# Performance work log

Hardware: AMD Instinct MI355X
Metric: run time of the kernel (lower is better)

## Reference

```python
import jax, jax.numpy as jnp
import numpy as np

B, S, H = 16, 4096, 1024

def setup_inputs() -> dict:
    key = jax.random.key(0)
    k1, k2, k3, k4 = jax.random.split(key, 4)
    hidden_states = jax.random.normal(k1, (B, S, H), dtype=jnp.float32)
    query_indices = jnp.sort(jax.random.randint(k2, (B, 2), 0, S), axis=1).astype(jnp.int64)
    attention_mask = jax.random.uniform(k3, (B,), dtype=jnp.float32)
    w = jax.random.normal(k4, (H,), dtype=jnp.float32) / jnp.sqrt(jnp.float32(H))
    return {"hidden_states": hidden_states, "query_indices": query_indices,
            "attention_mask": attention_mask, "w": w}

def reference(hidden_states, query_indices, attention_mask, w):
    # attention_mask is [B]; original broadcasts it over seq and hidden dims.
    hs = hidden_states * attention_mask[:, None, None]                  # [B,S,H]
    start = query_indices[:, 0]                                         # [B]
    end = query_indices[:, 1]                                           # [B]
    qlen = end - start                                                  # arange(start,end) length
    max_len = jnp.max(end + 1 - start)                                  # original pads to max(end-start+1)
    j = jnp.arange(S)                                                   # static padded query axis
    valid = j[None, :] < qlen[:, None]                                  # real gathered positions
    included = j[None, :] < max_len                                     # positions inside padded window
    idx = jnp.where(valid, start[:, None] + j[None, :], 0)              # [B,S]
    gathered = jnp.take_along_axis(hs, idx[:, :, None], axis=1)         # [B,S,H]
    gathered = gathered * valid[:, :, None].astype(hs.dtype)            # zero padded rows
    scores = jnp.einsum('bsh,h->bs', gathered, w)                       # padded-included rows score 0
    scores = jnp.where(included, scores, -jnp.inf)                      # beyond max_len: excluded
    attn = jax.nn.softmax(scores, axis=1)                               # [B,S]
    return jnp.einsum('bs,bsh->bh', attn, gathered)                     # [B,H]
```

## Files before the change

### kernel.cpp

```cpp
#include <hip/hip_runtime.h>
#include <math.h>

#define BB 16
#define SS 4096
#define HH 1024

__global__ __launch_bounds__(256) void score_kernel(
    const float* __restrict__ hidden,
    const int*   __restrict__ qidx,
    const float* __restrict__ mask,
    const float* __restrict__ w,
    float*       __restrict__ scores)
{
    const int b     = blockIdx.y;
    const int start = qidx[2 * b];
    const int qlen  = qidx[2 * b + 1] - start;
    const int lane  = threadIdx.x & 63;
    const int wave  = threadIdx.x >> 6;
    const int j     = blockIdx.x * 4 + wave;
    if (blockIdx.x * 4 >= qlen) return;
    if (j >= qlen) return;

    const float4* row =
        (const float4*)(hidden + ((size_t)b * SS + start + j) * HH);
    const float4* wv = (const float4*)w;

    float acc = 0.f;
#pragma unroll
    for (int k = 0; k < 4; ++k) {
        float4 hv = row[lane + 64 * k];
        float4 wr = wv[lane + 64 * k];
        acc += hv.x * wr.x + hv.y * wr.y + hv.z * wr.z + hv.w * wr.w;
    }
#pragma unroll
    for (int off = 32; off > 0; off >>= 1)
        acc += __shfl_down(acc, off, 64);
    if (lane == 0) scores[b * SS + j] = acc * mask[b];
}

__global__ __launch_bounds__(256) void softmax_kernel(
    const int*   __restrict__ qidx,
    const float* __restrict__ mask,
    float*       __restrict__ scores,
    float*       __restrict__ out)
{
    const int b     = blockIdx.x;
    const int start = qidx[2 * b];
    const int qlen  = qidx[2 * b + 1] - start;

    int max_len = 0;
    for (int i = 0; i < BB; ++i) {
        int l = qidx[2 * i + 1] - qidx[2 * i];
        max_len = max(max_len, l);
    }
    max_len += 1;

    const int tid  = threadIdx.x;
    const int lane = tid & 63;
    const int wave = tid >> 6;

    ((float4*)out)[b * (HH / 4) + tid] = make_float4(0.f, 0.f, 0.f, 0.f);

    __shared__ float red[8];

    float m = -INFINITY;
    for (int j = tid; j < qlen; j += 256) m = fmaxf(m, scores[b * SS + j]);
#pragma unroll
    for (int off = 32; off > 0; off >>= 1)
        m = fmaxf(m, __shfl_down(m, off, 64));
    if (lane == 0) red[wave] = m;
    __syncthreads();
    if (tid == 0) {
        float mm = fmaxf(fmaxf(red[0], red[1]), fmaxf(red[2], red[3]));
        red[0] = fmaxf(mm, 0.f);
    }
    __syncthreads();
    m = red[0];
    __syncthreads();

    float s = 0.f;
    for (int j = tid; j < qlen; j += 256) s += __expf(scores[b * SS + j] - m);
#pragma unroll
    for (int off = 32; off > 0; off >>= 1) s += __shfl_down(s, off, 64);
    if (lane == 0) red[wave] = s;
    __syncthreads();
    if (tid == 0) {
        float denom = red[0] + red[1] + red[2] + red[3];
        denom += (float)(max_len - qlen) * __expf(-m);
        red[4] = mask[b] / denom;
    }
    __syncthreads();
    const float scale = red[4];

    for (int j = tid; j < qlen; j += 256)
        scores[b * SS + j] = __expf(scores[b * SS + j] - m) * scale;
}

__global__ __launch_bounds__(256) void agg_kernel(
    const float* __restrict__ hidden,
    const int*   __restrict__ qidx,
    const float* __restrict__ weights,
    float*       __restrict__ out)
{
    const int b     = blockIdx.y;
    const int start = qidx[2 * b];
    const int qlen  = qidx[2 * b + 1] - start;
    const int j0    = blockIdx.x * 16;
    if (j0 >= qlen) return;
    const int jend = min(j0 + 16, qlen);
    const int tid  = threadIdx.x;

    const float4* base =
        (const float4*)(hidden + ((size_t)b * SS + start) * HH) + tid;

    float4 acc = make_float4(0.f, 0.f, 0.f, 0.f);
#pragma unroll 4
    for (int j = j0; j < jend; ++j) {
        const float wt = weights[b * SS + j];
        float4 hv = base[(size_t)j * (HH / 4)];
        acc.x += wt * hv.x;
        acc.y += wt * hv.y;
        acc.z += wt * hv.z;
        acc.w += wt * hv.w;
    }
    float* o = out + b * HH + tid * 4;
    atomicAdd(o + 0, acc.x);
    atomicAdd(o + 1, acc.y);
    atomicAdd(o + 2, acc.z);
    atomicAdd(o + 3, acc.w);
}

extern "C" void kernel_launch(void* const* d_in, const int* in_sizes, int n_in,
                              void* d_out, int out_size, void* d_ws, size_t ws_size,
                              hipStream_t stream)
{
    const float* hidden = (const float*)d_in[0];
    const int*   qidx   = (const int*)d_in[1];
    const float* mask   = (const float*)d_in[2];
    const float* w      = (const float*)d_in[3];
    float*       out    = (float*)d_out;
    float*       scores = (float*)d_ws;

    score_kernel<<<dim3(SS / 4, BB), 256, 0, stream>>>(hidden, qidx, mask, w, scores);
    softmax_kernel<<<BB, 256, 0, stream>>>(qidx, mask, scores, out);
    agg_kernel<<<dim3(SS / 16, BB), 256, 0, stream>>>(hidden, qidx, scores, out);
}
```

Measured before the change: 345.9 us.

## Fuse scoring, softmax and aggregation into single-pass partial sums

Replaces the three-kernel score/softmax/aggregate pipeline with one pass. Each wave computes a row's score, exponentiates it and accumulates the weighted row and the denominator while the row is still in registers. A small second kernel then reduces the per-block partials. Hidden states are read once instead of twice and the atomics are removed. In exchange, the max subtraction in softmax is dropped, so very large scores could overflow, and the partials need extra workspace.

```diff
diff --git a/kernel.cpp b/kernel.cpp
--- a/kernel.cpp
+++ b/kernel.cpp
@@ -4,49 +4,90 @@
 #define BB 16
 #define SS 4096
 #define HH 1024
+#define CH 64
+#define NWB (CH * 4)
 
-__global__ __launch_bounds__(256) void score_kernel(
+__global__ __launch_bounds__(256) void pass1_kernel(
     const float* __restrict__ hidden,
     const int*   __restrict__ qidx,
     const float* __restrict__ mask,
     const float* __restrict__ w,
-    float*       __restrict__ scores)
+    float4*      __restrict__ pnum,
+    float*       __restrict__ pden)
 {
     const int b     = blockIdx.y;
     const int start = qidx[2 * b];
     const int qlen  = qidx[2 * b + 1] - start;
     const int lane  = threadIdx.x & 63;
     const int wave  = threadIdx.x >> 6;
-    const int j     = blockIdx.x * 4 + wave;
-    if (blockIdx.x * 4 >= qlen) return;
-    if (j >= qlen) return;
+    const int wid   = blockIdx.x * 4 + wave;
+    const float mb  = mask[b];
 
-    const float4* row =
-        (const float4*)(hidden + ((size_t)b * SS + start + j) * HH);
-    const float4* wv = (const float4*)w;
+    float4 wreg[4];
+#pragma unroll
+    for (int k = 0; k < 4; ++k)
+        wreg[k] = ((const float4*)w)[lane + 64 * k];
 
-    float acc = 0.f;
+    float4 acc[4];
 #pragma unroll
-    for (int k = 0; k < 4; ++k) {
-        float4 hv = row[lane + 64 * k];
-        float4 wr = wv[lane + 64 * k];
-        acc += hv.x * wr.x + hv.y * wr.y + hv.z * wr.z + hv.w * wr.w;
+    for (int k = 0; k < 4; ++k) acc[k] = make_float4(0.f, 0.f, 0.f, 0.f);
+    float dacc = 0.f;
+
+    for (int j = wid; j < qlen; j += NWB) {
+        const float4* row =
+            (const float4*)(hidden + ((size_t)b * SS + start + j) * HH);
+        float4 hv[4];
+        float s = 0.f;
+#pragma unroll
+        for (int k = 0; k < 4; ++k) {
+            hv[k] = row[lane + 64 * k];
+            s += hv[k].x * wreg[k].x + hv[k].y * wreg[k].y +
+                 hv[k].z * wreg[k].z + hv[k].w * wreg[k].w;
+        }
+#pragma unroll
+        for (int off = 32; off > 0; off >>= 1)
+            s += __shfl_down(s, off, 64);
+        s = __shfl(s, 0, 64);
+        const float e = __expf(s * mb);
+        dacc += e;
+#pragma unroll
+        for (int k = 0; k < 4; ++k) {
+            acc[k].x += e * hv[k].x;
+            acc[k].y += e * hv[k].y;
+            acc[k].z += e * hv[k].z;
+            acc[k].w += e * hv[k].w;
+        }
     }
+
+    __shared__ float4 lred[4][256];
 #pragma unroll
-    for (int off = 32; off > 0; off >>= 1)
-        acc += __shfl_down(acc, off, 64);
-    if (lane == 0) scores[b * SS + j] = acc * mask[b];
+    for (int k = 0; k < 4; ++k)
+        lred[wave][lane + 64 * k] = acc[k];
+
+    __shared__ float dred[4];
+    if (lane == 0) dred[wave] = dacc;
+    __syncthreads();
+
+    const int t = threadIdx.x;
+    float4 s0 = lred[0][t], s1 = lred[1][t], s2 = lred[2][t], s3 = lred[3][t];
+    float4 sum = make_float4(s0.x + s1.x + s2.x + s3.x,
+                             s0.y + s1.y + s2.y + s3.y,
+                             s0.z + s1.z + s2.z + s3.z,
+                             s0.w + s1.w + s2.w + s3.w);
+    pnum[((size_t)b * CH + blockIdx.x) * 256 + t] = sum;
+    if (t == 0)
+        pden[b * CH + blockIdx.x] = dred[0] + dred[1] + dred[2] + dred[3];
 }
 
-__global__ __launch_bounds__(256) void softmax_kernel(
-    const int*   __restrict__ qidx,
-    const float* __restrict__ mask,
-    float*       __restrict__ scores,
-    float*       __restrict__ out)
+__global__ __launch_bounds__(256) void pass2_kernel(
+    const int*    __restrict__ qidx,
+    const float*  __restrict__ mask,
+    const float4* __restrict__ pnum,
+    const float*  __restrict__ pden,
+    float4*       __restrict__ out)
 {
-    const int b     = blockIdx.x;
-    const int start = qidx[2 * b];
-    const int qlen  = qidx[2 * b + 1] - start;
+    const int b = blockIdx.x;
+    const int t = threadIdx.x;
 
     int max_len = 0;
     for (int i = 0; i < BB; ++i) {
@@ -54,80 +95,20 @@
         max_len = max(max_len, l);
     }
     max_len += 1;
+    const int qlen = qidx[2 * b + 1] - qidx[2 * b];
 
-    const int tid  = threadIdx.x;
-    const int lane = tid & 63;
-    const int wave = tid >> 6;
-
-    ((float4*)out)[b * (HH / 4) + tid] = make_float4(0.f, 0.f, 0.f, 0.f);
-
-    __shared__ float red[8];
-
-    float m = -INFINITY;
-    for (int j = tid; j < qlen; j += 256) m = fmaxf(m, scores[b * SS + j]);
-#pragma unroll
-    for (int off = 32; off > 0; off >>= 1)
-        m = fmaxf(m, __shfl_down(m, off, 64));
-    if (lane == 0) red[wave] = m;
-    __syncthreads();
-    if (tid == 0) {
-        float mm = fmaxf(fmaxf(red[0], red[1]), fmaxf(red[2], red[3]));
-        red[0] = fmaxf(mm, 0.f);
+    float4 sum = make_float4(0.f, 0.f, 0.f, 0.f);
+    float den = 0.f;
+#pragma unroll 8
+    for (int c = 0; c < CH; ++c) {
+        float4 p = pnum[((size_t)b * CH + c) * 256 + t];
+        sum.x += p.x; sum.y += p.y; sum.z += p.z; sum.w += p.w;
+        den += pden[b * CH + c];
     }
-    __syncthreads();
-    m = red[0];
-    __syncthreads();
-
-    float s = 0.f;
-    for (int j = tid; j < qlen; j += 256) s += __expf(scores[b * SS + j] - m);
-#pragma unroll
-    for (int off = 32; off > 0; off >>= 1) s += __shfl_down(s, off, 64);
-    if (lane == 0) red[wave] = s;
-    __syncthreads();
-    if (tid == 0) {
-        float denom = red[0] + red[1] + red[2] + red[3];
-        denom += (float)(max_len - qlen) * __expf(-m);
-        red[4] = mask[b] / denom;
-    }
-    __syncthreads();
-    const float scale = red[4];
-
-    for (int j = tid; j < qlen; j += 256)
-        scores[b * SS + j] = __expf(scores[b * SS + j] - m) * scale;
-}
-
-__global__ __launch_bounds__(256) void agg_kernel(
-    const float* __restrict__ hidden,
-    const int*   __restrict__ qidx,
-    const float* __restrict__ weights,
-    float*       __restrict__ out)
-{
-    const int b     = blockIdx.y;
-    const int start = qidx[2 * b];
-    const int qlen  = qidx[2 * b + 1] - start;
-    const int j0    = blockIdx.x * 16;
-    if (j0 >= qlen) return;
-    const int jend = min(j0 + 16, qlen);
-    const int tid  = threadIdx.x;
-
-    const float4* base =
-        (const float4*)(hidden + ((size_t)b * SS + start) * HH) + tid;
-
-    float4 acc = make_float4(0.f, 0.f, 0.f, 0.f);
-#pragma unroll 4
-    for (int j = j0; j < jend; ++j) {
-        const float wt = weights[b * SS + j];
-        float4 hv = base[(size_t)j * (HH / 4)];
-        acc.x += wt * hv.x;
-        acc.y += wt * hv.y;
-        acc.z += wt * hv.z;
-        acc.w += wt * hv.w;
-    }
-    float* o = out + b * HH + tid * 4;
-    atomicAdd(o + 0, acc.x);
-    atomicAdd(o + 1, acc.y);
-    atomicAdd(o + 2, acc.z);
-    atomicAdd(o + 3, acc.w);
+    den += (float)(max_len - qlen);
+    const float scale = mask[b] / den;
+    out[b * 256 + t] = make_float4(sum.x * scale, sum.y * scale,
+                                   sum.z * scale, sum.w * scale);
 }
 
 extern "C" void kernel_launch(void* const* d_in, const int* in_sizes, int n_in,
@@ -138,10 +119,11 @@
     const int*   qidx   = (const int*)d_in[1];
     const float* mask   = (const float*)d_in[2];
     const float* w      = (const float*)d_in[3];
-    float*       out    = (float*)d_out;
-    float*       scores = (float*)d_ws;
 
-    score_kernel<<<dim3(SS / 4, BB), 256, 0, stream>>>(hidden, qidx, mask, w, scores);
-    softmax_kernel<<<BB, 256, 0, stream>>>(qidx, mask, scores, out);
-    agg_kernel<<<dim3(SS / 16, BB), 256, 0, stream>>>(hidden, qidx, scores, out);
+    float4* pnum = (float4*)d_ws;
+    float*  pden = (float*)((char*)d_ws + (size_t)BB * CH * 256 * 16);
+    float4* out  = (float4*)d_out;
+
+    pass1_kernel<<<dim3(CH, BB), 256, 0, stream>>>(hidden, qidx, mask, w, pnum, pden);
+    pass2_kernel<<<BB, 256, 0, stream>>>(qidx, mask, pnum, pden, out);
 }
```

New measurement: 314.1 us. 9.2% less time.
